# Kernel optimization log

Hardware: AMD Instinct MI355X
Metric: run time of the kernel (lower is better)

Reference implementation:

```python
import jax, jax.numpy as jnp
import numpy as np

B, N = 32, 2048
W_POINT, W_CHAMFER, W_STRUCT = 1.0, 5.0, 2.0
BIG = 1e10  # finite sentinel for masked-out distances
EPS = 1e-12


def setup_inputs() -> dict:
    key = jax.random.key(0)
    k1, k2, k3, k4, k5 = jax.random.split(key, 5)
    pred_xy = jax.random.normal(k1, (B, N, 2), dtype=jnp.float32)
    pred_v = jax.random.bernoulli(k2, 0.95, (B, N, 1)).astype(jnp.float32)
    tgt_xy = jax.random.normal(k3, (B, N, 2), dtype=jnp.float32)
    tgt_v = jax.random.bernoulli(k4, 0.95, (B, N, 1)).astype(jnp.float32)
    pred = jnp.concatenate([pred_xy, pred_v], axis=-1)
    target = jnp.concatenate([tgt_xy, tgt_v], axis=-1)
    skeleton_mask = jax.random.bernoulli(k5, 0.1, (B, N, 2)).astype(jnp.float32)
    return {"pred": pred, "target": target, "skeleton_mask": skeleton_mask}


def _skeleton_loss(pred, target, skeleton_mask):
    dt = pred.dtype
    tv = target[..., 2] == 1.0              # [B,N] valid target points
    vm = tv[..., None].astype(dt)           # [B,N,1]

    # masked MSE over coordinates (mean over ALL B*N*2 elements, as torch.mean)
    coord_err = (pred[..., :2] - target[..., :2]) * vm
    loss_point = jnp.mean(coord_err ** 2)

    # chamfer distance with validity masking (vectorized over batch)
    pv = pred[..., 2] == 1.0                # [B,N] valid pred points
    P, T = pred[..., :2], target[..., :2]
    d2 = (jnp.sum(P * P, -1)[:, :, None] + jnp.sum(T * T, -1)[:, None, :]
          - 2.0 * jnp.einsum('bnd,bmd->bnm', P, T))       # [B,Np,Nt]
    d = jnp.sqrt(jnp.maximum(d2, EPS))
    pvf = pv.astype(dt)
    tvf = tv.astype(dt)
    # pred -> target: min over valid target cols, mean over valid pred rows
    min_p = jnp.min(jnp.where(tv[:, None, :], d, BIG), axis=2)   # [B,Np]
    cnt_p = jnp.sum(pvf, axis=1)
    mean_p = jnp.sum(min_p * pvf, axis=1) / jnp.maximum(cnt_p, 1.0)
    # target -> pred
    min_t = jnp.min(jnp.where(pv[:, None, :], jnp.swapaxes(d, 1, 2), BIG), axis=2)
    cnt_t = jnp.sum(tvf, axis=1)
    mean_t = jnp.sum(min_t * tvf, axis=1) / jnp.maximum(cnt_t, 1.0)
    both = (cnt_p > 0) & (cnt_t > 0)
    chamfer_b = jnp.where(both, (mean_p + mean_t) * 0.5, 0.0)
    loss_chamfer = jnp.sum(chamfer_b) / B

    # structural point loss
    structure_mask = jnp.clip(skeleton_mask[..., 0] + skeleton_mask[..., 1], 0.0, 1.0)[..., None]
    total_mask = structure_mask * vm
    struct_err = (pred[..., :2] - target[..., :2]) * total_mask
    loss_structure = jnp.where(jnp.sum(total_mask) > 0, jnp.mean(struct_err ** 2), 0.0)

    total = W_POINT * loss_point + W_CHAMFER * loss_chamfer + W_STRUCT * loss_structure
    vis = jnp.zeros((), dtype=dt)
    # [skeleton_total_loss, skeleton_point_loss, skeleton_visibility_loss, skeleton_shape_loss]
    return jnp.stack([total, loss_point, vis, loss_chamfer])


def reference(pred, target, skeleton_mask):
    return _skeleton_loss(pred, target, skeleton_mask)
```

## Files before the change

kernel.cpp:

```cpp
#include <hip/hip_runtime.h>
#include <math.h>

#define BB 32
#define NN 2048
#define TB 256
#define QT 8
#define RCH 16
#define MCH (NN / RCH)
#define TB2 512


__device__ __forceinline__ float wred(float v) {
#pragma unroll
    for (int o = 32; o > 0; o >>= 1) v += __shfl_down(v, o, 64);
    return v;
}

__global__ __launch_bounds__(256) void k1_chamfer(
    const float* __restrict__ pred, const float* __restrict__ tgt,
    float* __restrict__ part, float* __restrict__ out)
{
    __shared__ float sa[MCH], sb[MCH], sc[MCH];

    const int tid  = threadIdx.x;
    const int b    = blockIdx.y;
    const int role = blockIdx.z & 1;
    const int rc   = blockIdx.z >> 1;

    if (b == 0 && blockIdx.z == 0 && tid < 4) out[tid] = 0.0f;

    const float* q = role ? tgt : pred;
    const float* r = role ? pred : tgt;
    const float* rb = r + ((size_t)b * NN + (size_t)rc * MCH) * 3;

    if (tid < MCH) {
        float rx = rb[3 * tid + 0];
        float ry = rb[3 * tid + 1];
        float rv = rb[3 * tid + 2];
        if (rv != 1.0f) { rx = 1.0e9f; ry = 1.0e9f; }
        sa[tid] = -2.0f * rx;
        sb[tid] = -2.0f * ry;
        sc[tid] = fmaf(rx, rx, ry * ry);
    }
    __syncthreads();

    const float* qb_ = q + (size_t)b * NN * 3;
    float px[QT], py[QT], mn[QT];
#pragma unroll
    for (int j = 0; j < QT; j++) {
        int qi = tid + j * TB;
        px[j] = qb_[3 * qi + 0];
        py[j] = qb_[3 * qi + 1];
        mn[j] = 3.4e38f;
    }

#pragma unroll 2
    for (int m = 0; m < MCH; m += 8) {
        float4 a0 = *(const float4*)&sa[m], a1 = *(const float4*)&sa[m + 4];
        float4 b0 = *(const float4*)&sb[m], b1 = *(const float4*)&sb[m + 4];
        float4 c0 = *(const float4*)&sc[m], c1 = *(const float4*)&sc[m + 4];
#pragma unroll
        for (int j = 0; j < QT; j++) {
            float s0 = fmaf(px[j], a0.x, fmaf(py[j], b0.x, c0.x));
            float s1 = fmaf(px[j], a0.y, fmaf(py[j], b0.y, c0.y));
            float s2 = fmaf(px[j], a0.z, fmaf(py[j], b0.z, c0.z));
            float s3 = fmaf(px[j], a0.w, fmaf(py[j], b0.w, c0.w));
            float s4 = fmaf(px[j], a1.x, fmaf(py[j], b1.x, c1.x));
            float s5 = fmaf(px[j], a1.y, fmaf(py[j], b1.y, c1.y));
            float s6 = fmaf(px[j], a1.z, fmaf(py[j], b1.z, c1.z));
            float s7 = fmaf(px[j], a1.w, fmaf(py[j], b1.w, c1.w));
            float u = fminf(fminf(s0, s1), s2);
            float v = fminf(fminf(s3, s4), s5);
            float w = fminf(fminf(s6, s7), mn[j]);
            mn[j] = fminf(fminf(u, v), w);
        }
    }

#pragma unroll
    for (int j = 0; j < QT; j++) {
        int qi = tid + j * TB;
        float qn = fmaf(px[j], px[j], py[j] * py[j]);
        part[((size_t)rc * (2 * BB) + role * BB + b) * NN + qi] = qn + mn[j];
    }
}

__global__ __launch_bounds__(TB2) void k2_final(
    const float* __restrict__ pred, const float* __restrict__ tgt,
    const float* __restrict__ smask, const float* __restrict__ part,
    float* __restrict__ out)
{
    __shared__ float sred[7][8];
    const int tid = threadIdx.x;
    const int b   = blockIdx.x;

    float a0 = 0, a1 = 0, a2 = 0, a3 = 0, a4 = 0, a5 = 0, a6 = 0;

#pragma unroll
    for (int j = 0; j < NN / TB2; j++) {
        int qi = tid + j * TB2;
        float m = 3.4e38f;
#pragma unroll
        for (int k = 0; k < RCH; k++)
            m = fminf(m, part[((size_t)k * (2 * BB) + b) * NN + qi]);

        const float* qp = pred + ((size_t)b * NN + qi) * 3;
        float qvf = (qp[2] == 1.0f) ? 1.0f : 0.0f;
        a0 += sqrtf(fmaxf(m, 1e-12f)) * qvf;
        a1 += qvf;

        const float* tp = tgt + ((size_t)b * NN + qi) * 3;
        float vm = (tp[2] == 1.0f) ? 1.0f : 0.0f;
        float dx = qp[0] - tp[0], dy = qp[1] - tp[1];
        float e2 = fmaf(dx, dx, dy * dy);
        float s0 = smask[((size_t)b * NN + qi) * 2 + 0];
        float s1 = smask[((size_t)b * NN + qi) * 2 + 1];
        float tm = fminf(fmaxf(s0 + s1, 0.0f), 1.0f) * vm;
        a2 += e2 * vm;
        a3 += e2 * tm;
        a4 += tm;
    }

#pragma unroll
    for (int j = 0; j < NN / TB2; j++) {
        int qi = tid + j * TB2;
        float m = 3.4e38f;
#pragma unroll
        for (int k = 0; k < RCH; k++)
            m = fminf(m, part[((size_t)k * (2 * BB) + BB + b) * NN + qi]);

        const float* qp = tgt + ((size_t)b * NN + qi) * 3;
        float qvf = (qp[2] == 1.0f) ? 1.0f : 0.0f;
        a5 += sqrtf(fmaxf(m, 1e-12f)) * qvf;
        a6 += qvf;
    }

    float v[7] = {a0, a1, a2, a3, a4, a5, a6};
    const int wave = tid >> 6, lane = tid & 63;
#pragma unroll
    for (int i = 0; i < 7; i++) {
        float rv = wred(v[i]);
        if (lane == 0) sred[i][wave] = rv;
    }
    __syncthreads();

    if (tid == 0) {
        float s[7];
#pragma unroll
        for (int i = 0; i < 7; i++) {
            float acc = 0.0f;
#pragma unroll
            for (int w = 0; w < TB2 / 64; w++) acc += sred[i][w];
            s[i] = acc;
        }
        float sp = s[0], cp = s[1], spt = s[2], sst = s[3];
        float st_ = s[5], ct = s[6];
        float mp = sp / fmaxf(cp, 1.0f);
        float mt = st_ / fmaxf(ct, 1.0f);
        float ch = (cp > 0.0f && ct > 0.0f) ? 0.5f * (mp + mt) : 0.0f;

        const float denom = (float)BB * (float)NN * 2.0f;
        float lp = spt / denom;
        float ls = sst / denom;
        float lc = ch / (float)BB;

        atomicAdd(&out[0], lp + 5.0f * lc + 2.0f * ls);
        atomicAdd(&out[1], lp);
        atomicAdd(&out[3], lc);
    }
}

extern "C" void kernel_launch(void* const* d_in, const int* in_sizes, int n_in,
                              void* d_out, int out_size, void* d_ws, size_t ws_size,
                              hipStream_t stream)
{
    const float* pred  = (const float*)d_in[0];
    const float* tgt   = (const float*)d_in[1];
    const float* smask = (const float*)d_in[2];
    float* out = (float*)d_out;
    float* part = (float*)d_ws;

    k1_chamfer<<<dim3(1, BB, 2 * RCH), TB, 0, stream>>>(pred, tgt, part, out);
    k2_final<<<dim3(BB), TB2, 0, stream>>>(pred, tgt, smask, part, out);
}
```

Measured before the change: 80.60 us.

## Split final reduction into wide partial kernel plus tiny finalizer, vectorize k1 loads/stores

The final reduction, previously 32 blocks of 512 threads, becomes a 256-block partial kernel with one point per thread, followed by a single-wave finalizer that writes the outputs directly instead of using atomics. In the chamfer kernel each thread now owns 8 contiguous query points, so query loads and partial-min stores use float4. The goal is to fill more of the GPU during the reduction phase and make memory accesses coalesced and vectorized, at the cost of one extra kernel launch and an extra workspace buffer.

```diff
diff --git a/kernel.cpp b/kernel.cpp
--- a/kernel.cpp
+++ b/kernel.cpp
@@ -7,7 +7,6 @@
 #define QT 8
 #define RCH 16
 #define MCH (NN / RCH)
-#define TB2 512
 
 
 __device__ __forceinline__ float wred(float v) {
@@ -16,9 +15,9 @@
     return v;
 }
 
-__global__ __launch_bounds__(256) void k1_chamfer(
+__global__ __launch_bounds__(TB) void k1_chamfer(
     const float* __restrict__ pred, const float* __restrict__ tgt,
-    float* __restrict__ part, float* __restrict__ out)
+    float* __restrict__ part)
 {
     __shared__ float sa[MCH], sb[MCH], sc[MCH];
 
@@ -27,12 +26,24 @@
     const int role = blockIdx.z & 1;
     const int rc   = blockIdx.z >> 1;
 
-    if (b == 0 && blockIdx.z == 0 && tid < 4) out[tid] = 0.0f;
-
     const float* q = role ? tgt : pred;
     const float* r = role ? pred : tgt;
+
+    const float* qb_ = q + (size_t)b * NN * 3;
+    float f[24];
+    const float4* qv = (const float4*)(qb_ + (size_t)tid * (QT * 3));
+#pragma unroll
+    for (int i = 0; i < 6; i++) ((float4*)f)[i] = qv[i];
+
+    float px[QT], py[QT], mn[QT];
+#pragma unroll
+    for (int j = 0; j < QT; j++) {
+        px[j] = f[3 * j + 0];
+        py[j] = f[3 * j + 1];
+        mn[j] = 3.4e38f;
+    }
+
     const float* rb = r + ((size_t)b * NN + (size_t)rc * MCH) * 3;
-
     if (tid < MCH) {
         float rx = rb[3 * tid + 0];
         float ry = rb[3 * tid + 1];
@@ -43,16 +54,6 @@
         sc[tid] = fmaf(rx, rx, ry * ry);
     }
     __syncthreads();
-
-    const float* qb_ = q + (size_t)b * NN * 3;
-    float px[QT], py[QT], mn[QT];
-#pragma unroll
-    for (int j = 0; j < QT; j++) {
-        int qi = tid + j * TB;
-        px[j] = qb_[3 * qi + 0];
-        py[j] = qb_[3 * qi + 1];
-        mn[j] = 3.4e38f;
-    }
 
 #pragma unroll 2
     for (int m = 0; m < MCH; m += 8) {
@@ -76,63 +77,53 @@
         }
     }
 
+    float o[QT];
 #pragma unroll
-    for (int j = 0; j < QT; j++) {
-        int qi = tid + j * TB;
-        float qn = fmaf(px[j], px[j], py[j] * py[j]);
-        part[((size_t)rc * (2 * BB) + role * BB + b) * NN + qi] = qn + mn[j];
-    }
+    for (int j = 0; j < QT; j++)
+        o[j] = fmaf(px[j], px[j], py[j] * py[j]) + mn[j];
+
+    float4* po = (float4*)&part[((size_t)rc * (2 * BB) + (size_t)role * BB + b) * NN
+                                + (size_t)tid * QT];
+    po[0] = make_float4(o[0], o[1], o[2], o[3]);
+    po[1] = make_float4(o[4], o[5], o[6], o[7]);
 }
 
-__global__ __launch_bounds__(TB2) void k2_final(
+__global__ __launch_bounds__(TB) void k2a_partial(
     const float* __restrict__ pred, const float* __restrict__ tgt,
     const float* __restrict__ smask, const float* __restrict__ part,
-    float* __restrict__ out)
+    float* __restrict__ partial)
 {
-    __shared__ float sred[7][8];
+    __shared__ float sred[7][4];
     const int tid = threadIdx.x;
-    const int b   = blockIdx.x;
+    const int c   = blockIdx.x;
+    const int b   = blockIdx.y;
+    const int qi  = c * TB + tid;
 
-    float a0 = 0, a1 = 0, a2 = 0, a3 = 0, a4 = 0, a5 = 0, a6 = 0;
+    float m0 = 3.4e38f, m1 = 3.4e38f;
+#pragma unroll
+    for (int k = 0; k < RCH; k++)
+        m0 = fminf(m0, part[((size_t)k * (2 * BB) + b) * NN + qi]);
+#pragma unroll
+    for (int k = 0; k < RCH; k++)
+        m1 = fminf(m1, part[((size_t)k * (2 * BB) + BB + b) * NN + qi]);
 
-#pragma unroll
-    for (int j = 0; j < NN / TB2; j++) {
-        int qi = tid + j * TB2;
-        float m = 3.4e38f;
-#pragma unroll
-        for (int k = 0; k < RCH; k++)
-            m = fminf(m, part[((size_t)k * (2 * BB) + b) * NN + qi]);
+    const float* qp = pred + ((size_t)b * NN + qi) * 3;
+    const float* tp = tgt  + ((size_t)b * NN + qi) * 3;
+    const float2 sm = *(const float2*)&smask[((size_t)b * NN + qi) * 2];
 
-        const float* qp = pred + ((size_t)b * NN + qi) * 3;
-        float qvf = (qp[2] == 1.0f) ? 1.0f : 0.0f;
-        a0 += sqrtf(fmaxf(m, 1e-12f)) * qvf;
-        a1 += qvf;
+    float pvf = (qp[2] == 1.0f) ? 1.0f : 0.0f;
+    float vm  = (tp[2] == 1.0f) ? 1.0f : 0.0f;
 
-        const float* tp = tgt + ((size_t)b * NN + qi) * 3;
-        float vm = (tp[2] == 1.0f) ? 1.0f : 0.0f;
-        float dx = qp[0] - tp[0], dy = qp[1] - tp[1];
-        float e2 = fmaf(dx, dx, dy * dy);
-        float s0 = smask[((size_t)b * NN + qi) * 2 + 0];
-        float s1 = smask[((size_t)b * NN + qi) * 2 + 1];
-        float tm = fminf(fmaxf(s0 + s1, 0.0f), 1.0f) * vm;
-        a2 += e2 * vm;
-        a3 += e2 * tm;
-        a4 += tm;
-    }
-
-#pragma unroll
-    for (int j = 0; j < NN / TB2; j++) {
-        int qi = tid + j * TB2;
-        float m = 3.4e38f;
-#pragma unroll
-        for (int k = 0; k < RCH; k++)
-            m = fminf(m, part[((size_t)k * (2 * BB) + BB + b) * NN + qi]);
-
-        const float* qp = tgt + ((size_t)b * NN + qi) * 3;
-        float qvf = (qp[2] == 1.0f) ? 1.0f : 0.0f;
-        a5 += sqrtf(fmaxf(m, 1e-12f)) * qvf;
-        a6 += qvf;
-    }
+    float a0 = sqrtf(fmaxf(m0, 1e-12f)) * pvf;
+    float a1 = pvf;
+    float dx = qp[0] - tp[0], dy = qp[1] - tp[1];
+    float e2 = fmaf(dx, dx, dy * dy);
+    float tm = fminf(fmaxf(sm.x + sm.y, 0.0f), 1.0f) * vm;
+    float a2 = e2 * vm;
+    float a3 = e2 * tm;
+    float a4 = tm;
+    float a5 = sqrtf(fmaxf(m1, 1e-12f)) * vm;
+    float a6 = vm;
 
     float v[7] = {a0, a1, a2, a3, a4, a5, a6};
     const int wave = tid >> 6, lane = tid & 63;
@@ -142,15 +133,26 @@
         if (lane == 0) sred[i][wave] = rv;
     }
     __syncthreads();
+    if (tid == 0) {
+        float* dst = partial + ((size_t)b * 8 + c) * 7;
+#pragma unroll
+        for (int i = 0; i < 7; i++)
+            dst[i] = sred[i][0] + sred[i][1] + sred[i][2] + sred[i][3];
+    }
+}
 
-    if (tid == 0) {
-        float s[7];
+__global__ __launch_bounds__(64) void k2b_final(
+    const float* __restrict__ partial, float* __restrict__ out)
+{
+    const int tid = threadIdx.x;
+    float lp = 0.0f, lc = 0.0f, ls = 0.0f;
+    if (tid < BB) {
+        float s[7] = {0, 0, 0, 0, 0, 0, 0};
 #pragma unroll
-        for (int i = 0; i < 7; i++) {
-            float acc = 0.0f;
+        for (int c = 0; c < 8; c++) {
+            const float* src = partial + ((size_t)tid * 8 + c) * 7;
 #pragma unroll
-            for (int w = 0; w < TB2 / 64; w++) acc += sred[i][w];
-            s[i] = acc;
+            for (int i = 0; i < 7; i++) s[i] += src[i];
         }
         float sp = s[0], cp = s[1], spt = s[2], sst = s[3];
         float st_ = s[5], ct = s[6];
@@ -159,13 +161,18 @@
         float ch = (cp > 0.0f && ct > 0.0f) ? 0.5f * (mp + mt) : 0.0f;
 
         const float denom = (float)BB * (float)NN * 2.0f;
-        float lp = spt / denom;
-        float ls = sst / denom;
-        float lc = ch / (float)BB;
-
-        atomicAdd(&out[0], lp + 5.0f * lc + 2.0f * ls);
-        atomicAdd(&out[1], lp);
-        atomicAdd(&out[3], lc);
+        lp = spt / denom;
+        ls = sst / denom;
+        lc = ch / (float)BB;
+    }
+    float t_lp = wred(lp);
+    float t_lc = wred(lc);
+    float t_ls = wred(ls);
+    if (tid == 0) {
+        out[0] = t_lp + 5.0f * t_lc + 2.0f * t_ls;
+        out[1] = t_lp;
+        out[2] = 0.0f;
+        out[3] = t_lc;
     }
 }
 
@@ -178,7 +185,9 @@
     const float* smask = (const float*)d_in[2];
     float* out = (float*)d_out;
     float* part = (float*)d_ws;
+    float* partial = (float*)((char*)d_ws + (size_t)RCH * 2 * BB * NN * 4);
 
-    k1_chamfer<<<dim3(1, BB, 2 * RCH), TB, 0, stream>>>(pred, tgt, part, out);
-    k2_final<<<dim3(BB), TB2, 0, stream>>>(pred, tgt, smask, part, out);
+    k1_chamfer<<<dim3(1, BB, 2 * RCH), TB, 0, stream>>>(pred, tgt, part);
+    k2a_partial<<<dim3(NN / TB, BB), TB, 0, stream>>>(pred, tgt, smask, part, partial);
+    k2b_final<<<dim3(1), 64, 0, stream>>>(partial, out);
 }
```

Measured after the change: 79.41 us, median of 2. Within noise of the previous version (-1.5%).
